# Kernel tuning notes

Measured on AMD Instinct MI355X. Metric: run time of the kernel, lower is better.

Reference implementation:

```python
import jax, jax.numpy as jnp
import numpy as np


def setup_inputs() -> dict:
    key = jax.random.key(0)
    k1, k2 = jax.random.split(key)
    B, H, W, D, C = 4, 128, 128, 128, 2
    image = jax.random.normal(k1, (B, H, W, D, C), dtype=jnp.float32)
    # near-identity affine so sampling is meaningful (localization-net output stand-in)
    theta = 0.1 * jax.random.normal(k2, (B, 3, 4), dtype=jnp.float32) + jnp.eye(3, 4, dtype=jnp.float32)[None]
    return {"image": image, "theta": theta}


def reference(image, theta):
    # Faithful port of SpatialTransformer._transform / _interpolate (incl. its
    # original index-flattening and z-weight (z1 - z0) conventions).
    B, H, W, D, C = image.shape
    oH, oW, oD = H, W, D  # downsample_factor = 1
    N = oH * oW * oD

    # _meshgrid: tf.meshgrid default 'xy' indexing -> shapes (oH, oW, oD)
    xl = jnp.linspace(-1.0, 1.0, oW)
    yl = jnp.linspace(-1.0, 1.0, oH)
    zl = jnp.linspace(-1.0, 1.0, oD)
    Xg, Yg, Zg = jnp.meshgrid(xl, yl, zl)
    grid = jnp.stack([Xg.ravel(), Yg.ravel(), Zg.ravel(), jnp.ones(N, jnp.float32)], 0)  # [4, N]

    tg = jnp.einsum('bij,jn->bin', theta.astype(jnp.float32), grid)  # [B, 3, N]
    x = tg[:, 0, :].reshape(-1)
    y = tg[:, 1, :].reshape(-1)
    z = tg[:, 2, :].reshape(-1)

    # map from [-1, 1] to pixel coords (original uses full extent, not extent-1)
    x = 0.5 * (x + 1.0) * W
    y = 0.5 * (y + 1.0) * H
    z = 0.5 * (z + 1.0) * D

    x0 = jnp.floor(x).astype(jnp.int32); x1 = x0 + 1
    y0 = jnp.floor(y).astype(jnp.int32); y1 = y0 + 1
    z0 = jnp.floor(z).astype(jnp.int32); z1 = z0 + 1
    x0 = jnp.clip(x0, 0, W - 1); x1 = jnp.clip(x1, 0, W - 1)
    y0 = jnp.clip(y0, 0, H - 1); y1 = jnp.clip(y1, 0, H - 1)
    z0 = jnp.clip(z0, 0, D - 1); z1 = jnp.clip(z1, 0, D - 1)

    base = jnp.repeat(jnp.arange(B, dtype=jnp.int32) * (H * W * D), N)  # [B*N]
    # original flat-index convention: base + y*W + z*W*H + x
    b00 = base + y0 * W + z0 * (W * H)
    b10 = base + y1 * W + z0 * (W * H)
    b01 = base + y0 * W + z1 * (W * H)
    b11 = base + y1 * W + z1 * (W * H)

    flat = image.reshape(-1, C).astype(jnp.float32)  # [B*H*W*D, C]
    pa = flat[b00 + x0]; pb = flat[b10 + x0]
    pc = flat[b00 + x1]; pd = flat[b10 + x1]
    pe = flat[b01 + x0]; pf = flat[b11 + x0]
    pg = flat[b01 + x1]; ph = flat[b11 + x1]

    x0f = x0.astype(jnp.float32); x1f = x1.astype(jnp.float32)
    y0f = y0.astype(jnp.float32); y1f = y1.astype(jnp.float32)
    z0f = z0.astype(jnp.float32); z1f = z1.astype(jnp.float32)

    wa = ((x1f - x) * (y1f - y) * (z1f - z))[:, None]
    wb = ((x1f - x) * (y - y0f) * (z1f - z))[:, None]
    wc = ((x - x0f) * (y1f - y) * (z1f - z))[:, None]
    wd = ((x - x0f) * (y - y0f) * (z1f - z))[:, None]
    we = ((x1f - x) * (y1f - y) * (z1f - z0f))[:, None]
    wf = ((x1f - x) * (y - y0f) * (z1f - z0f))[:, None]
    wg = ((x - x0f) * (y1f - y) * (z1f - z0f))[:, None]
    wh = ((x - x0f) * (y - y0f) * (z1f - z0f))[:, None]

    out = (wa * pa + wb * pb + wc * pc + wd * pd
           + we * pe + wf * pf + wg * pg + wh * ph)  # [B*N, C]
    return out.reshape(B, oH, oW, oD, C)
```

## Files before the change

### kernel.cpp

```cpp
#include <hip/hip_runtime.h>
#include <math.h>

#define BN 4
#define HN 128
#define WN 128
#define DN 128

__global__ __launch_bounds__(256) void st_trilerp_kernel(
    const float* __restrict__ image,
    const float* __restrict__ theta,
    float* __restrict__ out)
{
    const int bi = blockIdx.z;
    const int b  = bi >> 7;
    const int i  = bi & (HN - 1);
    const int j0 = blockIdx.y << 5;
    const int k0 = blockIdx.x << 4;

    const int tid = threadIdx.x;
    const int jj  = tid & 31;
    const int kg  = tid >> 5;
    const int j   = j0 + jj;
    const int kb  = k0 + (kg << 1);

    const double step = 2.0 / 127.0;
    const double X = (j == WN - 1) ? 1.0 : (double)j * step - 1.0;
    const double Y = (i == HN - 1) ? 1.0 : (double)i * step - 1.0;

    const float* th = theta + b * 12;
    const double t0 = (double)th[0], t1 = (double)th[1], t2  = (double)th[2],  t3  = (double)th[3];
    const double t4 = (double)th[4], t5 = (double)th[5], t6  = (double)th[6],  t7  = (double)th[7];
    const double t8 = (double)th[8], t9 = (double)th[9], t10 = (double)th[10], t11 = (double)th[11];

    const double KST = 128.0 / 127.0;
    const double Px = t2  * KST, Qx = fma(64.0, (t0*X + t1*Y) + t3  - t2,  64.0);
    const double Py = t6  * KST, Qy = fma(64.0, (t4*X + t5*Y) + t7  - t6,  64.0);
    const double Pz = t10 * KST, Qz = fma(64.0, (t8*X + t9*Y) + t11 - t10, 64.0);

    const int base = b * (HN * WN * DN);
    const float2* __restrict__ img2 = (const float2*)image;

    int   r00[2], r10[2], r01[2], r11[2];
    float wxL[2], wxH[2], wy0[2], wy1[2], wz0[2], wzA[2];

#pragma unroll
    for (int c = 0; c < 2; ++c) {
        const double kd = (double)(kb + c);
        const double x = fma(Px, kd, Qx);
        const double y = fma(Py, kd, Qy);
        const double z = fma(Pz, kd, Qz);

        const double xf = floor(x), yf = floor(y), zf = floor(z);
        const int x0u = (int)xf, y0u = (int)yf, z0u = (int)zf;
        const int x0 = min(max(x0u,     0), WN - 1);
        const int x1 = min(max(x0u + 1, 0), WN - 1);
        const int y0 = min(max(y0u,     0), HN - 1);
        const int y1 = min(max(y0u + 1, 0), HN - 1);
        const int z0 = min(max(z0u,     0), DN - 1);
        const int z1 = min(max(z0u + 1, 0), DN - 1);

        const float xs = (float)x, ys = (float)y, zs = (float)z;
        const float wx0f = (float)x1 - xs, wx1f = xs - (float)x0;
        wy0[c] = (float)y1 - ys;  wy1[c] = ys - (float)y0;
        wz0[c] = (float)z1 - zs;  wzA[c] = (float)(z1 - z0);

        const int xb  = min(x0, WN - 2);
        const bool lo0 = (x0 == xb), lo1 = (x1 == xb);
        wxL[c] = (lo0 ? wx0f : 0.0f) + (lo1 ? wx1f : 0.0f);
        wxH[c] = (lo0 ? 0.0f : wx0f) + (lo1 ? 0.0f : wx1f);

        const int rb = base + (y0 << 7) + (z0 << 14) + xb;
        const int dy = (y1 - y0) << 7;
        const int dz = (z1 - z0) << 14;
        r00[c] = rb;
        r10[c] = rb + dy;
        r01[c] = rb + dz;
        r11[c] = rb + dy + dz;
    }

#define GLOAD16(dst, ptr) \
    asm volatile("global_load_dwordx4 %0, %1, off" : "=v"(dst) : "v"(ptr))
    float4 q00[2], q10[2], q01[2], q11[2];
    GLOAD16(q00[0], img2 + r00[0]);
    GLOAD16(q10[0], img2 + r10[0]);
    GLOAD16(q01[0], img2 + r01[0]);
    GLOAD16(q11[0], img2 + r11[0]);
    GLOAD16(q00[1], img2 + r00[1]);
    GLOAD16(q10[1], img2 + r10[1]);
    GLOAD16(q01[1], img2 + r01[1]);
    GLOAD16(q11[1], img2 + r11[1]);

    asm volatile("s_waitcnt vmcnt(0)" ::: "memory");
    __builtin_amdgcn_sched_barrier(0);

    float ox[2], oy[2];
#pragma unroll
    for (int c = 0; c < 2; ++c) {
        const float g00x = wxL[c]*q00[c].x + wxH[c]*q00[c].z;
        const float g00y = wxL[c]*q00[c].y + wxH[c]*q00[c].w;
        const float g10x = wxL[c]*q10[c].x + wxH[c]*q10[c].z;
        const float g10y = wxL[c]*q10[c].y + wxH[c]*q10[c].w;
        const float g01x = wxL[c]*q01[c].x + wxH[c]*q01[c].z;
        const float g01y = wxL[c]*q01[c].y + wxH[c]*q01[c].w;
        const float g11x = wxL[c]*q11[c].x + wxH[c]*q11[c].z;
        const float g11y = wxL[c]*q11[c].y + wxH[c]*q11[c].w;

        const float h0x = wy0[c]*g00x + wy1[c]*g10x;
        const float h0y = wy0[c]*g00y + wy1[c]*g10y;
        const float h1x = wy0[c]*g01x + wy1[c]*g11x;
        const float h1y = wy0[c]*g01y + wy1[c]*g11y;

        ox[c] = wz0[c]*h0x + wzA[c]*h1x;
        oy[c] = wz0[c]*h0y + wzA[c]*h1y;
    }

    __shared__ float2 tile[16][33];
    const int kk = kg << 1;
    tile[kk + 0][jj] = make_float2(ox[0], oy[0]);
    tile[kk + 1][jj] = make_float2(ox[1], oy[1]);
    __syncthreads();

    const int row = tid >> 3;
    const int q   = tid & 7;
    const float2 a = tile[2*q + 0][row];
    const float2 bb = tile[2*q + 1][row];
    const int oidx = (bi * WN + (j0 + row)) * DN + k0 + 2*q;
    *(float4*)((float2*)out + oidx) = make_float4(a.x, a.y, bb.x, bb.y);
}

extern "C" void kernel_launch(void* const* d_in, const int* in_sizes, int n_in,
                              void* d_out, int out_size, void* d_ws, size_t ws_size,
                              hipStream_t stream) {
    const float* image = (const float*)d_in[0];
    const float* theta = (const float*)d_in[1];
    float* out = (float*)d_out;

    dim3 grid(DN / 16, WN / 32, BN * HN);
    st_trilerp_kernel<<<grid, 256, 0, stream>>>(image, theta, out);
}
```

Before: 138.8 us.

## Swizzle workgroups across XCDs, split load wait, use nontemporal output stores

Flattens the 3D grid to 1D and remaps block ids so consecutive tiles go to the same XCD (orig&7 selects a contiguous chunk of work). This keeps neighbouring gather footprints in the same L2. It also splits the vmcnt wait so the first voxel's combine overlaps the second voxel's loads, and makes the output store nontemporal so it does not pollute the cache. The remap assumes 8 XCDs with round-robin dispatch.

```diff
diff --git a/kernel.cpp b/kernel.cpp
--- a/kernel.cpp
+++ b/kernel.cpp
@@ -6,16 +6,28 @@
 #define WN 128
 #define DN 128
 
+
+typedef float f32x4 __attribute__((ext_vector_type(4)));
+
+#define GLOAD16(dst, ptr) \
+    asm volatile("global_load_dwordx4 %0, %1, off" : "=v"(dst) : "v"(ptr))
+#define VMWAIT(n) do { \
+    asm volatile("s_waitcnt vmcnt(" #n ")" ::: "memory"); \
+    __builtin_amdgcn_sched_barrier(0); } while (0)
+
 __global__ __launch_bounds__(256) void st_trilerp_kernel(
     const float* __restrict__ image,
     const float* __restrict__ theta,
     float* __restrict__ out)
 {
-    const int bi = blockIdx.z;
+    const int orig = blockIdx.x;
+    const int wgid = ((orig & 7) << 11) | (orig >> 3);
+    const int bi  = wgid >> 5;
+    const int rem = wgid & 31;
     const int b  = bi >> 7;
     const int i  = bi & (HN - 1);
-    const int j0 = blockIdx.y << 5;
-    const int k0 = blockIdx.x << 4;
+    const int j0 = (rem >> 3) << 5;
+    const int k0 = (rem & 7) << 4;
 
     const int tid = threadIdx.x;
     const int jj  = tid & 31;
@@ -78,8 +90,6 @@
         r11[c] = rb + dy + dz;
     }
 
-#define GLOAD16(dst, ptr) \
-    asm volatile("global_load_dwordx4 %0, %1, off" : "=v"(dst) : "v"(ptr))
     float4 q00[2], q10[2], q01[2], q11[2];
     GLOAD16(q00[0], img2 + r00[0]);
     GLOAD16(q10[0], img2 + r10[0]);
@@ -90,42 +100,39 @@
     GLOAD16(q01[1], img2 + r01[1]);
     GLOAD16(q11[1], img2 + r11[1]);
 
-    asm volatile("s_waitcnt vmcnt(0)" ::: "memory");
-    __builtin_amdgcn_sched_barrier(0);
-
-    float ox[2], oy[2];
-#pragma unroll
-    for (int c = 0; c < 2; ++c) {
-        const float g00x = wxL[c]*q00[c].x + wxH[c]*q00[c].z;
-        const float g00y = wxL[c]*q00[c].y + wxH[c]*q00[c].w;
-        const float g10x = wxL[c]*q10[c].x + wxH[c]*q10[c].z;
-        const float g10y = wxL[c]*q10[c].y + wxH[c]*q10[c].w;
-        const float g01x = wxL[c]*q01[c].x + wxH[c]*q01[c].z;
-        const float g01y = wxL[c]*q01[c].y + wxH[c]*q01[c].w;
-        const float g11x = wxL[c]*q11[c].x + wxH[c]*q11[c].z;
-        const float g11y = wxL[c]*q11[c].y + wxH[c]*q11[c].w;
-
-        const float h0x = wy0[c]*g00x + wy1[c]*g10x;
-        const float h0y = wy0[c]*g00y + wy1[c]*g10y;
-        const float h1x = wy0[c]*g01x + wy1[c]*g11x;
-        const float h1y = wy0[c]*g01y + wy1[c]*g11y;
-
-        ox[c] = wz0[c]*h0x + wzA[c]*h1x;
-        oy[c] = wz0[c]*h0y + wzA[c]*h1y;
-    }
-
     __shared__ float2 tile[16][33];
     const int kk = kg << 1;
-    tile[kk + 0][jj] = make_float2(ox[0], oy[0]);
-    tile[kk + 1][jj] = make_float2(ox[1], oy[1]);
+
+#define COMBINE(c) do { \
+        const float g00x = wxL[c]*q00[c].x + wxH[c]*q00[c].z; \
+        const float g00y = wxL[c]*q00[c].y + wxH[c]*q00[c].w; \
+        const float g10x = wxL[c]*q10[c].x + wxH[c]*q10[c].z; \
+        const float g10y = wxL[c]*q10[c].y + wxH[c]*q10[c].w; \
+        const float g01x = wxL[c]*q01[c].x + wxH[c]*q01[c].z; \
+        const float g01y = wxL[c]*q01[c].y + wxH[c]*q01[c].w; \
+        const float g11x = wxL[c]*q11[c].x + wxH[c]*q11[c].z; \
+        const float g11y = wxL[c]*q11[c].y + wxH[c]*q11[c].w; \
+        const float h0x = wy0[c]*g00x + wy1[c]*g10x; \
+        const float h0y = wy0[c]*g00y + wy1[c]*g10y; \
+        const float h1x = wy0[c]*g01x + wy1[c]*g11x; \
+        const float h1y = wy0[c]*g01y + wy1[c]*g11y; \
+        tile[kk + c][jj] = make_float2(wz0[c]*h0x + wzA[c]*h1x, \
+                                       wz0[c]*h0y + wzA[c]*h1y); \
+    } while (0)
+
+    VMWAIT(4); COMBINE(0);
+    VMWAIT(0); COMBINE(1);
+#undef COMBINE
+
     __syncthreads();
 
     const int row = tid >> 3;
     const int q   = tid & 7;
-    const float2 a = tile[2*q + 0][row];
+    const float2 a  = tile[2*q + 0][row];
     const float2 bb = tile[2*q + 1][row];
     const int oidx = (bi * WN + (j0 + row)) * DN + k0 + 2*q;
-    *(float4*)((float2*)out + oidx) = make_float4(a.x, a.y, bb.x, bb.y);
+    f32x4 val; val.x = a.x; val.y = a.y; val.z = bb.x; val.w = bb.y;
+    __builtin_nontemporal_store(val, (f32x4*)((float2*)out + oidx));
 }
 
 extern "C" void kernel_launch(void* const* d_in, const int* in_sizes, int n_in,
@@ -135,6 +142,5 @@
     const float* theta = (const float*)d_in[1];
     float* out = (float*)d_out;
 
-    dim3 grid(DN / 16, WN / 32, BN * HN);
-    st_trilerp_kernel<<<grid, 256, 0, stream>>>(image, theta, out);
+    st_trilerp_kernel<<<dim3(16384), 256, 0, stream>>>(image, theta, out);
 }
```

New measurement: 138.3 us. About the same (-0.4%).
